# Optimization experiments

Measured on AMD Instinct MI355X. Metric: run time of the kernel, lower is better.

The kernel has to match this reference:

```python
import jax, jax.numpy as jnp
import numpy as np

SEQ_LEN = 256
VOCAB_SIZE = 96
MAX_WEIGHT = 2.0
EPS = 1e-8


def setup_inputs() -> dict:
    key = jax.random.key(0)
    k1, k2 = jax.random.split(key)
    batch = 2048
    # char values in 0..VOCAB_SIZE; 0 means masked/hidden, 1..V are chars
    char_values = jax.random.randint(k1, (batch, SEQ_LEN), 0, VOCAB_SIZE + 1, dtype=jnp.int32)
    # nn.init.uniform_(raw_weights, -1.0, 1.0)
    raw_weights = jax.random.uniform(
        k2, (VOCAB_SIZE, SEQ_LEN * VOCAB_SIZE), minval=-1.0, maxval=1.0, dtype=jnp.float32
    )
    return {"char_values": char_values, "raw_weights": raw_weights}


def reference(char_values, raw_weights):
    # Sparse gather-and-reduce equivalent of the dense one-hot broadcast:
    # only the seq_len fired dendrites per sample contribute to the log-sum.
    revealed = (char_values > 0).astype(raw_weights.dtype)        # (B, S)
    dend_idx = jnp.arange(SEQ_LEN, dtype=jnp.int32)[None, :] * VOCAB_SIZE \
        + jnp.maximum(char_values - 1, 0)                         # (B, S)

    # Bounded positive weights, clamped, in log space: (V, D)
    log_w = jnp.log(jnp.maximum(MAX_WEIGHT * jax.nn.sigmoid(raw_weights), EPS))

    # Gather log-weights of fired dendrites for every output class: (B, S, V)
    gathered = log_w.T[dend_idx]
    log_sum = jnp.einsum("bsv,bs->bv", gathered, revealed)        # (B, V)

    n_active = jnp.maximum(jnp.sum(revealed, axis=1, keepdims=True), 1.0)  # (B, 1)
    logits = jnp.exp(log_sum / n_active)                          # geometric mean
    return logits
```

## Files before the change

kernel.cpp:

```cpp
#include <hip/hip_runtime.h>
#include <hip/hip_bf16.h>

#define SEQ_LEN 256
#define VOCAB 96
#define D_TOTAL (SEQ_LEN * VOCAB)
#define BATCH 2048
#define ZROW_OFF (D_TOTAL * VOCAB)

typedef _Float16 half_t;
typedef _Float16 half2_t __attribute__((ext_vector_type(2)));

__global__ __launch_bounds__(256) void build_lwT_kernel(
    const float* __restrict__ raw, half_t* __restrict__ lwT) {
    __shared__ float tile[32][33];
    const int d0 = blockIdx.x * 32;
    const int v0 = blockIdx.y * 32;
    const int tx = threadIdx.x;
    const int ty = threadIdx.y;
    const int t = ty * 32 + tx;

    if (blockIdx.x == 0 && blockIdx.y == 0 && t < VOCAB)
        lwT[ZROW_OFF + t] = (half_t)0.0f;

#pragma unroll
    for (int j = 0; j < 4; ++j) {
        const int v = v0 + ty + j * 8;
        const float x = raw[v * D_TOTAL + d0 + tx];
        const float w = 2.0f / (1.0f + __expf(-x));
        tile[ty + j * 8][tx] = __logf(fmaxf(w, 1e-8f));
    }
    __syncthreads();
#pragma unroll
    for (int j = 0; j < 4; ++j) {
        const int d = d0 + ty + j * 8;
        lwT[d * VOCAB + v0 + tx] = (half_t)tile[tx][ty + j * 8];
    }
}

__global__ __launch_bounds__(384, 8) void gather_kernel(
    const int* __restrict__ cv, const half_t* __restrict__ lwT,
    float* __restrict__ out) {
    __shared__ int s_off[SEQ_LEN];
    __shared__ float s_acc[8][VOCAB];
    __shared__ int s_cnt[8];
    const int t = threadIdx.x;
    const int b = blockIdx.x;

    if (t < SEQ_LEN) {
        const int c = cv[b * SEQ_LEN + t];
        s_off[t] = (c > 0) ? (t * VOCAB + (c - 1)) * VOCAB : ZROW_OFF;
    }
    __syncthreads();

    const int chunk = t / 48;
    const int vp = t - chunk * 48;
    const int s0 = chunk * 32;

    float acc0 = 0.0f, acc1 = 0.0f;
    int cnt = 0;
#pragma unroll 16
    for (int i = 0; i < 32; ++i) {
        const int off = s_off[s0 + i];
        const half2_t w = *(const half2_t*)(lwT + off + 2 * vp);
        acc0 += (float)w.x;
        acc1 += (float)w.y;
        cnt += (off != ZROW_OFF);
    }
    s_acc[chunk][2 * vp] = acc0;
    s_acc[chunk][2 * vp + 1] = acc1;
    if (vp == 0) s_cnt[chunk] = cnt;
    __syncthreads();

    if (t < VOCAB) {
        float a = 0.0f;
        int n = 0;
#pragma unroll
        for (int ch = 0; ch < 8; ++ch) { a += s_acc[ch][t]; n += s_cnt[ch]; }
        out[b * VOCAB + t] = __expf(a / fmaxf((float)n, 1.0f));
    }
}

extern "C" void kernel_launch(void* const* d_in, const int* in_sizes, int n_in,
                              void* d_out, int out_size, void* d_ws, size_t ws_size,
                              hipStream_t stream) {
    const int* cv = (const int*)d_in[0];
    const float* raw = (const float*)d_in[1];
    float* out = (float*)d_out;
    half_t* lwT = (half_t*)d_ws;

    dim3 g1(D_TOTAL / 32, VOCAB / 32);
    dim3 b1(32, 8);
    build_lwT_kernel<<<g1, b1, 0, stream>>>(raw, lwT);

    gather_kernel<<<BATCH, 384, 0, stream>>>(cv, lwT, out);
}
```

Baseline: 77.40 us.

## Widen gather loads to 16-byte half8 vectors and count revealed chars via ballot

The gather kernel now loads 8 halfs (16 bytes) per thread per sequence position instead of 2. The 384 threads are remapped to 32 chunks of 8 positions times 12 vocab groups, so each row of 96 log-weights is fetched by 12 wide loads and fewer memory instructions are issued. The per-chunk active count is replaced by a wavefront ballot and popcount when the inputs are loaded. The cost is a larger shared partial-sum array (32 by 97) and a 32-way final reduction per output, plus more registers per thread.

```diff
diff --git a/kernel.cpp b/kernel.cpp
--- a/kernel.cpp
+++ b/kernel.cpp
@@ -8,7 +8,7 @@
 #define ZROW_OFF (D_TOTAL * VOCAB)
 
 typedef _Float16 half_t;
-typedef _Float16 half2_t __attribute__((ext_vector_type(2)));
+typedef _Float16 half8_t __attribute__((ext_vector_type(8)));
 
 __global__ __launch_bounds__(256) void build_lwT_kernel(
     const float* __restrict__ raw, half_t* __restrict__ lwT) {
@@ -41,42 +41,42 @@
     const int* __restrict__ cv, const half_t* __restrict__ lwT,
     float* __restrict__ out) {
     __shared__ int s_off[SEQ_LEN];
-    __shared__ float s_acc[8][VOCAB];
-    __shared__ int s_cnt[8];
+    __shared__ float s_acc[32][97];
+    __shared__ int s_cntw[4];
     const int t = threadIdx.x;
     const int b = blockIdx.x;
 
-    if (t < SEQ_LEN) {
-        const int c = cv[b * SEQ_LEN + t];
+    int c = 0;
+    if (t < SEQ_LEN) c = cv[b * SEQ_LEN + t];
+    const unsigned long long bal = __ballot(c > 0);
+    if ((t & 63) == 0 && t < SEQ_LEN) s_cntw[t >> 6] = __popcll(bal);
+    if (t < SEQ_LEN)
         s_off[t] = (c > 0) ? (t * VOCAB + (c - 1)) * VOCAB : ZROW_OFF;
-    }
     __syncthreads();
 
-    const int chunk = t / 48;
-    const int vp = t - chunk * 48;
-    const int s0 = chunk * 32;
+    const int chunk = t / 12;
+    const int vq = t - chunk * 12;
+    const int s0 = chunk * 8;
+    const half_t* __restrict__ lwp = lwT + 8 * vq;
 
-    float acc0 = 0.0f, acc1 = 0.0f;
-    int cnt = 0;
-#pragma unroll 16
-    for (int i = 0; i < 32; ++i) {
+    float acc[8] = {0, 0, 0, 0, 0, 0, 0, 0};
+#pragma unroll
+    for (int i = 0; i < 8; ++i) {
         const int off = s_off[s0 + i];
-        const half2_t w = *(const half2_t*)(lwT + off + 2 * vp);
-        acc0 += (float)w.x;
-        acc1 += (float)w.y;
-        cnt += (off != ZROW_OFF);
+        const half8_t w = *(const half8_t*)(lwp + off);
+#pragma unroll
+        for (int j = 0; j < 8; ++j) acc[j] += (float)w[j];
     }
-    s_acc[chunk][2 * vp] = acc0;
-    s_acc[chunk][2 * vp + 1] = acc1;
-    if (vp == 0) s_cnt[chunk] = cnt;
+#pragma unroll
+    for (int j = 0; j < 8; ++j) s_acc[chunk][8 * vq + j] = acc[j];
     __syncthreads();
 
     if (t < VOCAB) {
         float a = 0.0f;
-        int n = 0;
 #pragma unroll
-        for (int ch = 0; ch < 8; ++ch) { a += s_acc[ch][t]; n += s_cnt[ch]; }
-        out[b * VOCAB + t] = __expf(a / fmaxf((float)n, 1.0f));
+        for (int ch = 0; ch < 32; ++ch) a += s_acc[ch][t];
+        const float n = (float)(s_cntw[0] + s_cntw[1] + s_cntw[2] + s_cntw[3]);
+        out[b * VOCAB + t] = __expf(a / fmaxf(n, 1.0f));
     }
 }
 
```

Measured after the change: 76.49 us. Within noise of the previous version (-1.2%).
